# Kernel optimization log

Hardware: AMD Instinct MI355X
Metric: run time of the kernel (lower is better)

## Reference

```python
import jax, jax.numpy as jnp
import numpy as np

N_NODES = 100000
N_EDGES = 1600000
IN_C, HID_C, OUT_C = 64, 64, 32


def setup_inputs() -> dict:
    key = jax.random.key(0)
    ks = jax.random.split(key, 10)
    return {
        "x": jax.random.normal(ks[0], (N_NODES, IN_C), dtype=jnp.float32),
        "edge_index": jax.random.randint(ks[1], (2, N_EDGES), 0, N_NODES, dtype=jnp.int32),
        "W_l": jax.random.normal(ks[2], (IN_C, HID_C), dtype=jnp.float32) * 0.1,
        "W_r": jax.random.normal(ks[3], (IN_C, HID_C), dtype=jnp.float32) * 0.1,
        "b1": jax.random.normal(ks[4], (HID_C,), dtype=jnp.float32) * 0.1,
        "W_g": jax.random.normal(ks[5], (HID_C, OUT_C), dtype=jnp.float32) * 0.1,
        "att_src": jax.random.normal(ks[6], (OUT_C,), dtype=jnp.float32) * 0.1,
        "att_dst": jax.random.normal(ks[7], (OUT_C,), dtype=jnp.float32) * 0.1,
        "b2": jax.random.normal(ks[8], (OUT_C,), dtype=jnp.float32) * 0.1,
    }


def _gnn(x, edge_index, W_l, W_r, b1, W_g, att_src, att_dst, b2):
    n = x.shape[0]
    src, dst = edge_index[0], edge_index[1]

    # --- SAGEConv: mean neighbor aggregation + root transform ---
    deg = jax.ops.segment_sum(jnp.ones_like(src, dtype=x.dtype), dst, num_segments=n)
    agg = jax.ops.segment_sum(x[src], dst, num_segments=n)  # [N, IN_C]
    agg = agg / jnp.maximum(deg, 1.0)[:, None]
    h = agg @ W_l + b1 + x @ W_r
    h = jax.nn.relu(h)
    # dropout(p=0.5) is identity in eval mode

    # --- GATConv (heads=1), with self-loops (PyG default) ---
    loop = jnp.arange(n, dtype=src.dtype)
    s = jnp.concatenate([src, loop])
    d = jnp.concatenate([dst, loop])
    z = h @ W_g                      # [N, OUT_C]
    a_s = z @ att_src                # [N] per-node source score
    a_d = z @ att_dst                # [N] per-node dest score
    e = jax.nn.leaky_relu(a_s[s] + a_d[d], negative_slope=0.2)  # [E+N]
    # segment softmax over edges grouped by destination node
    m = jax.ops.segment_max(e, d, num_segments=n)
    ex = jnp.exp(e - m[d])
    denom = jax.ops.segment_sum(ex, d, num_segments=n)
    alpha = ex / denom[d]
    out = jax.ops.segment_sum(alpha[:, None] * z[s], d, num_segments=n) + b2

    return jax.nn.log_softmax(out, axis=1)


def reference(x, edge_index, W_l, W_r, b1, W_g, att_src, att_dst, b2):
    return _gnn(x, edge_index, W_l, W_r, b1, W_g, att_src, att_dst, b2)
```

## Files before the change

kernel.cpp:

```cpp
#include <hip/hip_runtime.h>
#include <cstdint>
#include <cstddef>


typedef unsigned short ushort_t;
typedef unsigned int uint_t;
typedef __attribute__((ext_vector_type(8))) short short8;
typedef __attribute__((ext_vector_type(4))) float f32x4;
typedef __attribute__((ext_vector_type(2))) float f32x2;

__device__ inline ushort_t f2bf(float f) {
    uint_t u = __float_as_uint(f);
    uint_t r = (u + 0x7fffu + ((u >> 16) & 1u)) >> 16;
    return (ushort_t)r;
}
__device__ inline uint_t pkbf(float a, float b) {
    return (uint_t)f2bf(a) | ((uint_t)f2bf(b) << 16);
}

#define PART_CHUNK 8192


__global__ __launch_bounds__(256) void k_pre(const float* __restrict__ x, ushort_t* __restrict__ xh,
                                             unsigned char* __restrict__ xq,
                                             const int* __restrict__ ei,
                                             int* __restrict__ cnt,
                                             const float* __restrict__ Wl, const float* __restrict__ Wr,
                                             const float* __restrict__ Wg,
                                             ushort_t* __restrict__ Wlrt, ushort_t* __restrict__ Wgt,
                                             unsigned char* __restrict__ zq,
                                             int n4, int E, int NB, int N, int nchunk) {
    __shared__ int h[512];
    int bid = blockIdx.x, tid = threadIdx.x;
    int idx = bid * 256 + tid;
    if (idx < n4) {
        float4 v = ((const float4*)x)[idx];
        ushort4 o = { f2bf(v.x), f2bf(v.y), f2bf(v.z), f2bf(v.w) };
        ((ushort4*)xh)[idx] = o;
        int r = 0;
        r = __builtin_amdgcn_cvt_pk_fp8_f32(v.x, v.y, r, false);
        r = __builtin_amdgcn_cvt_pk_fp8_f32(v.z, v.w, r, true);
        ((uint_t*)xq)[idx] = (uint_t)r;
    }
    if (bid < nchunk) {
        for (int b = tid; b < NB; b += 256) h[b] = 0;
        __syncthreads();
        int b0 = bid * PART_CHUNK;
        int b1 = min(b0 + PART_CHUNK, E);
        for (int j = b0 + tid; j < b1; j += 256) atomicAdd(&h[ei[E + j] >> 8], 1);
        __syncthreads();
        int* crow = cnt + (size_t)bid * NB;
        for (int b = tid; b < NB; b += 256) crow[b] = h[b];
    } else if (bid == nchunk) {
        if (tid < 16) ((uint_t*)(xq + (size_t)N * 64))[tid] = 0;
        if (tid < 8)  ((uint_t*)(zq + (size_t)N * 32))[tid] = 0;
    } else if (bid >= 512 && bid < 544) {
        int t = (bid - 512) * 256 + tid;
        int n = t >> 7, k = t & 127;
        float v = (k < 64) ? Wl[k * 64 + n] : Wr[(k - 64) * 64 + n];
        Wlrt[n * 128 + k] = f2bf(v);
        if (t < 32 * 64) {
            int n2 = t >> 6, k2 = t & 63;
            Wgt[n2 * 64 + k2] = f2bf(Wg[k2 * 32 + n2]);
        }
    }
}


__global__ __launch_bounds__(256) void k_part(const int* __restrict__ ei, const int* __restrict__ cnt,
                                              int* __restrict__ base, int* __restrict__ rowptr,
                                              uint_t* __restrict__ pairs, int E, int NB, int N,
                                              int nchunk) {
    __shared__ int tot_s[512];
    __shared__ int ofs[512];
    __shared__ int t[256];
    int tid = threadIdx.x, bid = blockIdx.x;
    for (int b = tid; b < NB; b += 256) {
        const int* col = cnt + b;
        int tsum = 0, moff = 0;
        int c = 0;
        for (; c + 16 <= nchunk; c += 16) {
            int v[16];
            #pragma unroll
            for (int k = 0; k < 16; ++k) v[k] = col[(size_t)(c + k) * NB];
            #pragma unroll
            for (int k = 0; k < 16; ++k) {
                tsum += v[k];
                moff += (c + k < bid) ? v[k] : 0;
            }
        }
        for (; c < nchunk; ++c) {
            int v = col[(size_t)c * NB];
            tsum += v;
            moff += (c < bid) ? v : 0;
        }
        tot_s[b] = tsum;
        ofs[b] = moff;
    }
    __syncthreads();
    int v0 = (2 * tid < NB) ? tot_s[2 * tid] : 0;
    int v1 = (2 * tid + 1 < NB) ? tot_s[2 * tid + 1] : 0;
    t[tid] = v0 + v1;
    __syncthreads();
    for (int off = 1; off < 256; off <<= 1) {
        int u = (tid >= off) ? t[tid - off] : 0;
        __syncthreads();
        t[tid] += u;
        __syncthreads();
    }
    int pairExcl = (tid > 0) ? t[tid - 1] : 0;
    if (2 * tid < NB) {
        ofs[2 * tid] += pairExcl;
        if (bid == 0) base[2 * tid] = pairExcl;
    }
    if (2 * tid + 1 < NB) {
        ofs[2 * tid + 1] += pairExcl + v0;
        if (bid == 0) base[2 * tid + 1] = pairExcl + v0;
    }
    if (bid == 0 && tid == 0) { base[NB] = E; rowptr[N] = E; }
    __syncthreads();
    int b0 = bid * PART_CHUNK;
    int b1 = min(b0 + PART_CHUNK, E);
    for (int j = b0 + tid; j < b1; j += 256) {
        int d = ei[E + j], s = ei[j];
        int p = atomicAdd(&ofs[d >> 8], 1);
        pairs[p] = (uint_t)s | ((uint_t)(d & 255) << 24);
    }
}


__global__ __launch_bounds__(256) void k_csr(const uint_t* __restrict__ pairs, const int* __restrict__ base,
                                             int* __restrict__ rowptr, int* __restrict__ csr, int N) {
    __shared__ int h[256];
    __shared__ int s[256];
    int b = blockIdx.x;
    int d0 = b << 8;
    int e0 = base[b], e1 = base[b + 1];
    int tid = threadIdx.x;
    h[tid] = 0;
    __syncthreads();
    for (int j = e0 + tid; j < e1; j += 256) atomicAdd(&h[pairs[j] >> 24], 1);
    __syncthreads();
    int v = h[tid];
    s[tid] = v;
    __syncthreads();
    for (int off = 1; off < 256; off <<= 1) {
        int u = (tid >= off) ? s[tid - off] : 0;
        __syncthreads();
        s[tid] += u;
        __syncthreads();
    }
    int excl = s[tid] - v;
    if (d0 + tid < N) rowptr[d0 + tid] = e0 + excl;
    __syncthreads();
    h[tid] = e0 + excl;
    __syncthreads();
    for (int j = e0 + tid; j < e1; j += 256) {
        uint_t p = pairs[j];
        int pos = atomicAdd(&h[p >> 24], 1);
        csr[pos] = (int)(p & 0xffffffu);
    }
}


__global__ __launch_bounds__(256) void k_gather(const int* __restrict__ rowptr, const int* __restrict__ csr,
                                                const unsigned char* __restrict__ xq,
                                                ushort_t* __restrict__ aggh, int N) {
    __shared__ int scr[256];
    int tid = threadIdx.x;
    int l = tid & 15, g = tid >> 4;
    int i = blockIdx.x * 16 + g;
    if (i >= N) return;
    int r0 = rowptr[i], r1 = rowptr[i + 1];
    int sub = l >> 3, lc = l & 7;
    const char* xb = (const char*)xq + lc * 8;
    float a0 = 0.f, a1 = 0.f, a2 = 0.f, a3 = 0.f;
    float a4 = 0.f, a5 = 0.f, a6 = 0.f, a7 = 0.f;
    for (int bb = r0; bb < r1; bb += 16) {
        int idx = bb + l;
        int src = (idx < r1) ? csr[idx] : N;
        scr[tid] = src << 6;
        uint4 q0 = *(const uint4*)&scr[g * 16 + 0];
        uint4 q1 = *(const uint4*)&scr[g * 16 + 4];
        uint4 q2 = *(const uint4*)&scr[g * 16 + 8];
        uint4 q3 = *(const uint4*)&scr[g * 16 + 12];
#define HSTEP(oa, ob) { \
        uint_t off = sub ? (ob) : (oa); \
        uint2 u = *(const uint2*)(xb + off); \
        f32x2 p0 = __builtin_amdgcn_cvt_pk_f32_fp8((int)u.x, false); \
        f32x2 p1 = __builtin_amdgcn_cvt_pk_f32_fp8((int)u.x, true); \
        f32x2 p2 = __builtin_amdgcn_cvt_pk_f32_fp8((int)u.y, false); \
        f32x2 p3 = __builtin_amdgcn_cvt_pk_f32_fp8((int)u.y, true); \
        a0 += p0.x; a1 += p0.y; a2 += p1.x; a3 += p1.y; \
        a4 += p2.x; a5 += p2.y; a6 += p3.x; a7 += p3.y; }
        HSTEP(q0.x, q0.y) HSTEP(q0.z, q0.w)
        HSTEP(q1.x, q1.y) HSTEP(q1.z, q1.w)
        HSTEP(q2.x, q2.y) HSTEP(q2.z, q2.w)
        HSTEP(q3.x, q3.y) HSTEP(q3.z, q3.w)
#undef HSTEP
    }
    a0 += __shfl_xor(a0, 8, 64); a1 += __shfl_xor(a1, 8, 64);
    a2 += __shfl_xor(a2, 8, 64); a3 += __shfl_xor(a3, 8, 64);
    a4 += __shfl_xor(a4, 8, 64); a5 += __shfl_xor(a5, 8, 64);
    a6 += __shfl_xor(a6, 8, 64); a7 += __shfl_xor(a7, 8, 64);
    if (sub == 0) {
        float dn = 1.0f / fmaxf((float)(r1 - r0), 1.0f);
        uint4 o = { pkbf(a0 * dn, a1 * dn), pkbf(a2 * dn, a3 * dn),
                    pkbf(a4 * dn, a5 * dn), pkbf(a6 * dn, a7 * dn) };
        *(uint4*)(aggh + (size_t)i * 64 + lc * 8) = o;
    }
}


__global__ __launch_bounds__(256) void k_gemm(const ushort_t* __restrict__ aggh, const ushort_t* __restrict__ xh,
                                              const ushort_t* __restrict__ Wlrt, const ushort_t* __restrict__ Wgt,
                                              const float* __restrict__ b1,
                                              const float* __restrict__ att_src, const float* __restrict__ att_dst,
                                              unsigned char* __restrict__ zq, float* __restrict__ a_s,
                                              float* __restrict__ a_d, int N) {
    __shared__ ushort_t Wls[64 * 136];
    __shared__ ushort_t Wgs[32 * 72];
    __shared__ ushort_t hs[64 * 136];
    int tid = threadIdx.x;
    for (int t = tid; t < 64 * 16; t += 256) {
        int n = t >> 4, cq = t & 15;
        *(uint4*)(&Wls[n * 136 + cq * 8]) = *(const uint4*)(&Wlrt[n * 128 + cq * 8]);
    }
    for (int t = tid; t < 32 * 8; t += 256) {
        int n = t >> 3, cq = t & 7;
        *(uint4*)(&Wgs[n * 72 + cq * 8]) = *(const uint4*)(&Wgt[n * 64 + cq * 8]);
    }
    __syncthreads();

    int w = tid >> 6, lane = tid & 63;
    int c = lane & 15, quad = lane >> 4;
    int m0 = blockIdx.x * 64 + w * 16;
    int row = m0 + c;
    bool rowok = row < N;

    f32x4 acc[4] = {};
    #pragma unroll
    for (int kk = 0; kk < 4; ++kk) {
        const ushort_t* Abase = (kk < 2) ? aggh : xh;
        int koff = (kk & 1) * 32 + quad * 8;
        short8 a = {};
        if (rowok) a = *(const short8*)(Abase + (size_t)row * 64 + koff);
        #pragma unroll
        for (int nb = 0; nb < 4; ++nb) {
            short8 b = *(const short8*)(&Wls[(nb * 16 + c) * 136 + kk * 32 + quad * 8]);
            acc[nb] = __builtin_amdgcn_mfma_f32_16x16x32_bf16(a, b, acc[nb], 0, 0, 0);
        }
    }
    ushort_t* hw = &hs[w * 16 * 136];
    #pragma unroll
    for (int nb = 0; nb < 4; ++nb) {
        float bb = b1[nb * 16 + c];
        #pragma unroll
        for (int r = 0; r < 4; ++r) {
            float h = acc[nb][r] + bb;
            hw[(quad * 4 + r) * 136 + nb * 16 + c] = f2bf(fmaxf(h, 0.f));
        }
    }
    f32x4 acc2[2] = {};
    #pragma unroll
    for (int kk = 0; kk < 2; ++kk) {
        short8 a = *(const short8*)(&hw[c * 136 + kk * 32 + quad * 8]);
        #pragma unroll
        for (int nb = 0; nb < 2; ++nb) {
            short8 b = *(const short8*)(&Wgs[(nb * 16 + c) * 72 + kk * 32 + quad * 8]);
            acc2[nb] = __builtin_amdgcn_mfma_f32_16x16x32_bf16(a, b, acc2[nb], 0, 0, 0);
        }
    }
    float as0 = att_src[c], as1 = att_src[16 + c];
    float ad0 = att_dst[c], ad1 = att_dst[16 + c];
    #pragma unroll
    for (int r = 0; r < 4; ++r) {
        int grow = m0 + quad * 4 + r;
        float z0 = acc2[0][r], z1 = acc2[1][r];
        float ps = z0 * as0 + z1 * as1;
        float pd = z0 * ad0 + z1 * ad1;
        #pragma unroll
        for (int off = 8; off; off >>= 1) {
            ps += __shfl_xor(ps, off, 64);
            pd += __shfl_xor(pd, off, 64);
        }
        if (grow < N) {
            int r8 = __builtin_amdgcn_cvt_pk_fp8_f32(z0, z1, 0, false);
            unsigned char* zrow = zq + (size_t)grow * 32;
            zrow[c] = (unsigned char)(r8 & 0xff);
            zrow[16 + c] = (unsigned char)((r8 >> 8) & 0xff);
            if (c == 0) { a_s[grow] = ps; a_d[grow] = pd; }
        }
    }
}


__global__ __launch_bounds__(256) void k_gat(const unsigned char* __restrict__ zq, const float* __restrict__ a_s,
                                             const float* __restrict__ a_d, const int* __restrict__ rowptr,
                                             const int* __restrict__ csr, const float* __restrict__ b2,
                                             float* __restrict__ out, int N) {
    __shared__ uint2 scr[256];
    int tid = threadIdx.x;
    int l = tid & 15, g = tid >> 4;
    int i = blockIdx.x * 16 + g;
    if (i >= N) return;
    int r0 = rowptr[i], r1 = rowptr[i + 1];
    float adi = a_d[i], asi = a_s[i];
    int sub = l >> 3, lc = l & 7;
    const char* zb = (const char*)zq + lc * 4;
    float a0 = 0.f, a1 = 0.f, a2 = 0.f, a3 = 0.f, dsum = 0.f;

    for (int bb = r0; bb < r1; bb += 16) {
        int idx = bb + l;
        bool valid = idx < r1;
        int s_l = valid ? csr[idx] : N;
        float w_l = 0.f;
        if (valid) {
            float e = a_s[s_l] + adi;
            e = fmaxf(e, 0.2f * e);
            w_l = __expf(e);
            dsum += w_l;
        }
        scr[tid] = make_uint2((uint_t)(s_l << 5), __float_as_uint(w_l));
        #pragma unroll
        for (int r = 0; r < 8; ++r) {
            uint4 q = *(const uint4*)&scr[g * 16 + r * 2];
            uint_t off = sub ? q.z : q.x;
            float w = __uint_as_float(sub ? q.w : q.y);
            uint_t u = *(const uint_t*)(zb + off);
            f32x2 p0 = __builtin_amdgcn_cvt_pk_f32_fp8((int)u, false);
            f32x2 p1 = __builtin_amdgcn_cvt_pk_f32_fp8((int)u, true);
            a0 += w * p0.x; a1 += w * p0.y;
            a2 += w * p1.x; a3 += w * p1.y;
        }
    }
    #pragma unroll
    for (int off = 8; off; off >>= 1) dsum += __shfl_xor(dsum, off, 64);
    a0 += __shfl_xor(a0, 8, 64); a1 += __shfl_xor(a1, 8, 64);
    a2 += __shfl_xor(a2, 8, 64); a3 += __shfl_xor(a3, 8, 64);
    float es = asi + adi; es = fmaxf(es, 0.2f * es);
    float wse = __expf(es);
    float denom = dsum + wse;
    uint_t us = *(const uint_t*)((const char*)zq + (size_t)i * 32 + lc * 4);
    f32x2 s0 = __builtin_amdgcn_cvt_pk_f32_fp8((int)us, false);
    f32x2 s1 = __builtin_amdgcn_cvt_pk_f32_fp8((int)us, true);
    a0 += wse * s0.x; a1 += wse * s0.y;
    a2 += wse * s1.x; a3 += wse * s1.y;

    float rden = 1.0f / denom;
    float o0 = a0 * rden + b2[lc * 4 + 0];
    float o1 = a1 * rden + b2[lc * 4 + 1];
    float o2 = a2 * rden + b2[lc * 4 + 2];
    float o3 = a3 * rden + b2[lc * 4 + 3];
    float m2 = fmaxf(fmaxf(o0, o1), fmaxf(o2, o3));
    #pragma unroll
    for (int off = 4; off; off >>= 1) m2 = fmaxf(m2, __shfl_xor(m2, off, 64));
    float ssum = __expf(o0 - m2) + __expf(o1 - m2) + __expf(o2 - m2) + __expf(o3 - m2);
    #pragma unroll
    for (int off = 4; off; off >>= 1) ssum += __shfl_xor(ssum, off, 64);
    float lg = m2 + __logf(ssum);
    if (sub == 0) {
        float4 r = { o0 - lg, o1 - lg, o2 - lg, o3 - lg };
        *(float4*)(out + (size_t)i * 32 + lc * 4) = r;
    }
}


extern "C" void kernel_launch(void* const* d_in, const int* in_sizes, int n_in,
                              void* d_out, int out_size, void* d_ws, size_t ws_size,
                              hipStream_t stream) {
    const float* x       = (const float*)d_in[0];
    const int*   ei      = (const int*)d_in[1];
    const float* Wl      = (const float*)d_in[2];
    const float* Wr      = (const float*)d_in[3];
    const float* b1      = (const float*)d_in[4];
    const float* Wg      = (const float*)d_in[5];
    const float* att_src = (const float*)d_in[6];
    const float* att_dst = (const float*)d_in[7];
    const float* b2      = (const float*)d_in[8];
    float* out = (float*)d_out;

    int N = in_sizes[0] / 64;
    int E = in_sizes[1] / 2;
    int NB = (N + 255) >> 8;
    int nchunk = (E + PART_CHUNK - 1) / PART_CHUNK;

    char* ws = (char*)d_ws;
    size_t off = 0;
    auto alloc = [&](size_t bytes) { size_t r = off; off += (bytes + 255) & ~(size_t)255; return r; };
    int* base      = (int*)(ws + alloc((size_t)(NB + 1) * 4));
    int* cnt       = (int*)(ws + alloc((size_t)nchunk * NB * 4));
    int* rowptr    = (int*)(ws + alloc((size_t)(N + 1) * 4));
    uint_t* pairs  = (uint_t*)(ws + alloc((size_t)E * 4));
    int* csr       = (int*)(ws + alloc((size_t)E * 4));
    ushort_t* xh   = (ushort_t*)(ws + alloc((size_t)N * 64 * 2));
    unsigned char* xq = (unsigned char*)(ws + alloc((size_t)(N + 1) * 64));
    ushort_t* aggh = (ushort_t*)(ws + alloc((size_t)N * 64 * 2));
    unsigned char* zq = (unsigned char*)(ws + alloc((size_t)(N + 1) * 32));
    float* a_s     = (float*)(ws + alloc((size_t)N * 4));
    float* a_d     = (float*)(ws + alloc((size_t)N * 4));
    ushort_t* Wlrt = (ushort_t*)(ws + alloc(64 * 128 * 2));
    ushort_t* Wgt  = (ushort_t*)(ws + alloc(32 * 64 * 2));

    int n4 = N * 64 / 4;
    int gpre = (n4 + 255) / 256;
    if (gpre < 545) gpre = 545;
    k_pre    <<<gpre, 256, 0, stream>>>(x, xh, xq, ei, cnt, Wl, Wr, Wg, Wlrt, Wgt, zq, n4, E, NB, N, nchunk);
    k_part   <<<nchunk, 256, 0, stream>>>(ei, cnt, base, rowptr, pairs, E, NB, N, nchunk);
    k_csr    <<<NB, 256, 0, stream>>>(pairs, base, rowptr, csr, N);
    k_gather <<<(N + 15) / 16, 256, 0, stream>>>(rowptr, csr, xq, aggh, N);
    k_gemm   <<<(N + 63) / 64, 256, 0, stream>>>(aggh, xh, Wlrt, Wgt, b1, att_src, att_dst, zq, a_s, a_d, N);
    k_gat    <<<(N + 15) / 16, 256, 0, stream>>>(zq, a_s, a_d, rowptr, csr, b2, out, N);
}
```

Baseline: 194.3 us.

## Fuse neighbor-mean gather into SAGE GEMM kernel via shared-memory aggregate

Merges the gather kernel into the GEMM kernel. Each 64-row block now computes its own neighbor means into shared memory and feeds them straight to the MFMA stage, removing the bf16 aggregate buffer and its global write and read, plus one launch. The cost is less parallelism in the gather phase: 64 nodes per block instead of 16, so there are four times fewer blocks. Load imbalance across degrees also now stalls the GEMM part of the same block.

```diff
diff --git a/kernel.cpp b/kernel.cpp
--- a/kernel.cpp
+++ b/kernel.cpp
@@ -163,65 +163,21 @@
 }
 
 
-__global__ __launch_bounds__(256) void k_gather(const int* __restrict__ rowptr, const int* __restrict__ csr,
-                                                const unsigned char* __restrict__ xq,
-                                                ushort_t* __restrict__ aggh, int N) {
-    __shared__ int scr[256];
-    int tid = threadIdx.x;
-    int l = tid & 15, g = tid >> 4;
-    int i = blockIdx.x * 16 + g;
-    if (i >= N) return;
-    int r0 = rowptr[i], r1 = rowptr[i + 1];
-    int sub = l >> 3, lc = l & 7;
-    const char* xb = (const char*)xq + lc * 8;
-    float a0 = 0.f, a1 = 0.f, a2 = 0.f, a3 = 0.f;
-    float a4 = 0.f, a5 = 0.f, a6 = 0.f, a7 = 0.f;
-    for (int bb = r0; bb < r1; bb += 16) {
-        int idx = bb + l;
-        int src = (idx < r1) ? csr[idx] : N;
-        scr[tid] = src << 6;
-        uint4 q0 = *(const uint4*)&scr[g * 16 + 0];
-        uint4 q1 = *(const uint4*)&scr[g * 16 + 4];
-        uint4 q2 = *(const uint4*)&scr[g * 16 + 8];
-        uint4 q3 = *(const uint4*)&scr[g * 16 + 12];
-#define HSTEP(oa, ob) { \
-        uint_t off = sub ? (ob) : (oa); \
-        uint2 u = *(const uint2*)(xb + off); \
-        f32x2 p0 = __builtin_amdgcn_cvt_pk_f32_fp8((int)u.x, false); \
-        f32x2 p1 = __builtin_amdgcn_cvt_pk_f32_fp8((int)u.x, true); \
-        f32x2 p2 = __builtin_amdgcn_cvt_pk_f32_fp8((int)u.y, false); \
-        f32x2 p3 = __builtin_amdgcn_cvt_pk_f32_fp8((int)u.y, true); \
-        a0 += p0.x; a1 += p0.y; a2 += p1.x; a3 += p1.y; \
-        a4 += p2.x; a5 += p2.y; a6 += p3.x; a7 += p3.y; }
-        HSTEP(q0.x, q0.y) HSTEP(q0.z, q0.w)
-        HSTEP(q1.x, q1.y) HSTEP(q1.z, q1.w)
-        HSTEP(q2.x, q2.y) HSTEP(q2.z, q2.w)
-        HSTEP(q3.x, q3.y) HSTEP(q3.z, q3.w)
-#undef HSTEP
-    }
-    a0 += __shfl_xor(a0, 8, 64); a1 += __shfl_xor(a1, 8, 64);
-    a2 += __shfl_xor(a2, 8, 64); a3 += __shfl_xor(a3, 8, 64);
-    a4 += __shfl_xor(a4, 8, 64); a5 += __shfl_xor(a5, 8, 64);
-    a6 += __shfl_xor(a6, 8, 64); a7 += __shfl_xor(a7, 8, 64);
-    if (sub == 0) {
-        float dn = 1.0f / fmaxf((float)(r1 - r0), 1.0f);
-        uint4 o = { pkbf(a0 * dn, a1 * dn), pkbf(a2 * dn, a3 * dn),
-                    pkbf(a4 * dn, a5 * dn), pkbf(a6 * dn, a7 * dn) };
-        *(uint4*)(aggh + (size_t)i * 64 + lc * 8) = o;
-    }
-}
-
-
-__global__ __launch_bounds__(256) void k_gemm(const ushort_t* __restrict__ aggh, const ushort_t* __restrict__ xh,
-                                              const ushort_t* __restrict__ Wlrt, const ushort_t* __restrict__ Wgt,
-                                              const float* __restrict__ b1,
-                                              const float* __restrict__ att_src, const float* __restrict__ att_dst,
-                                              unsigned char* __restrict__ zq, float* __restrict__ a_s,
-                                              float* __restrict__ a_d, int N) {
+__global__ __launch_bounds__(256) void k_gg(const int* __restrict__ rowptr, const int* __restrict__ csr,
+                                            const unsigned char* __restrict__ xq,
+                                            const ushort_t* __restrict__ xh,
+                                            const ushort_t* __restrict__ Wlrt, const ushort_t* __restrict__ Wgt,
+                                            const float* __restrict__ b1,
+                                            const float* __restrict__ att_src, const float* __restrict__ att_dst,
+                                            unsigned char* __restrict__ zq, float* __restrict__ a_s,
+                                            float* __restrict__ a_d, int N) {
     __shared__ ushort_t Wls[64 * 136];
     __shared__ ushort_t Wgs[32 * 72];
-    __shared__ ushort_t hs[64 * 136];
+    __shared__ ushort_t agg[64 * 72];
+    __shared__ __align__(16) char hsraw[64 * 136 * 2];
     int tid = threadIdx.x;
+    int blk = blockIdx.x;
+
     for (int t = tid; t < 64 * 16; t += 256) {
         int n = t >> 4, cq = t & 15;
         *(uint4*)(&Wls[n * 136 + cq * 8]) = *(const uint4*)(&Wlrt[n * 128 + cq * 8]);
@@ -230,21 +186,74 @@
         int n = t >> 3, cq = t & 7;
         *(uint4*)(&Wgs[n * 72 + cq * 8]) = *(const uint4*)(&Wgt[n * 64 + cq * 8]);
     }
-    __syncthreads();
-
+
+    {
+        int* scr = (int*)hsraw;
+        int l = tid & 15, g = tid >> 4;
+        int sub = l >> 3, lc = l & 7;
+        const char* xb = (const char*)xq + lc * 8;
+        #pragma unroll
+        for (int rep = 0; rep < 4; ++rep) {
+            int ilocal = rep * 16 + g;
+            int i = blk * 64 + ilocal;
+            if (i < N) {
+                int r0 = rowptr[i], r1 = rowptr[i + 1];
+                float a0 = 0.f, a1 = 0.f, a2 = 0.f, a3 = 0.f;
+                float a4 = 0.f, a5 = 0.f, a6 = 0.f, a7 = 0.f;
+                for (int bb = r0; bb < r1; bb += 16) {
+                    int idx = bb + l;
+                    int src = (idx < r1) ? csr[idx] : N;
+                    scr[tid] = src << 6;
+                    uint4 q0 = *(const uint4*)&scr[g * 16 + 0];
+                    uint4 q1 = *(const uint4*)&scr[g * 16 + 4];
+                    uint4 q2 = *(const uint4*)&scr[g * 16 + 8];
+                    uint4 q3 = *(const uint4*)&scr[g * 16 + 12];
+#define HSTEP(oa, ob) { \
+                    uint_t off = sub ? (ob) : (oa); \
+                    uint2 u = *(const uint2*)(xb + off); \
+                    f32x2 p0 = __builtin_amdgcn_cvt_pk_f32_fp8((int)u.x, false); \
+                    f32x2 p1 = __builtin_amdgcn_cvt_pk_f32_fp8((int)u.x, true); \
+                    f32x2 p2 = __builtin_amdgcn_cvt_pk_f32_fp8((int)u.y, false); \
+                    f32x2 p3 = __builtin_amdgcn_cvt_pk_f32_fp8((int)u.y, true); \
+                    a0 += p0.x; a1 += p0.y; a2 += p1.x; a3 += p1.y; \
+                    a4 += p2.x; a5 += p2.y; a6 += p3.x; a7 += p3.y; }
+                    HSTEP(q0.x, q0.y) HSTEP(q0.z, q0.w)
+                    HSTEP(q1.x, q1.y) HSTEP(q1.z, q1.w)
+                    HSTEP(q2.x, q2.y) HSTEP(q2.z, q2.w)
+                    HSTEP(q3.x, q3.y) HSTEP(q3.z, q3.w)
+#undef HSTEP
+                }
+                a0 += __shfl_xor(a0, 8, 64); a1 += __shfl_xor(a1, 8, 64);
+                a2 += __shfl_xor(a2, 8, 64); a3 += __shfl_xor(a3, 8, 64);
+                a4 += __shfl_xor(a4, 8, 64); a5 += __shfl_xor(a5, 8, 64);
+                a6 += __shfl_xor(a6, 8, 64); a7 += __shfl_xor(a7, 8, 64);
+                if (sub == 0) {
+                    float dn = 1.0f / fmaxf((float)(r1 - r0), 1.0f);
+                    uint4 o = { pkbf(a0 * dn, a1 * dn), pkbf(a2 * dn, a3 * dn),
+                                pkbf(a4 * dn, a5 * dn), pkbf(a6 * dn, a7 * dn) };
+                    *(uint4*)(&agg[ilocal * 72 + lc * 8]) = o;
+                }
+            }
+        }
+    }
+    __syncthreads();
+
+    ushort_t* hs = (ushort_t*)hsraw;
     int w = tid >> 6, lane = tid & 63;
     int c = lane & 15, quad = lane >> 4;
-    int m0 = blockIdx.x * 64 + w * 16;
+    int m0 = blk * 64 + w * 16;
     int row = m0 + c;
     bool rowok = row < N;
 
     f32x4 acc[4] = {};
     #pragma unroll
     for (int kk = 0; kk < 4; ++kk) {
-        const ushort_t* Abase = (kk < 2) ? aggh : xh;
         int koff = (kk & 1) * 32 + quad * 8;
         short8 a = {};
-        if (rowok) a = *(const short8*)(Abase + (size_t)row * 64 + koff);
+        if (rowok) {
+            if (kk < 2) a = *(const short8*)(&agg[(w * 16 + c) * 72 + koff]);
+            else        a = *(const short8*)(xh + (size_t)row * 64 + koff);
+        }
         #pragma unroll
         for (int nb = 0; nb < 4; ++nb) {
             short8 b = *(const short8*)(&Wls[(nb * 16 + c) * 136 + kk * 32 + quad * 8]);
@@ -395,7 +404,6 @@
     int* csr       = (int*)(ws + alloc((size_t)E * 4));
     ushort_t* xh   = (ushort_t*)(ws + alloc((size_t)N * 64 * 2));
     unsigned char* xq = (unsigned char*)(ws + alloc((size_t)(N + 1) * 64));
-    ushort_t* aggh = (ushort_t*)(ws + alloc((size_t)N * 64 * 2));
     unsigned char* zq = (unsigned char*)(ws + alloc((size_t)(N + 1) * 32));
     float* a_s     = (float*)(ws + alloc((size_t)N * 4));
     float* a_d     = (float*)(ws + alloc((size_t)N * 4));
@@ -405,10 +413,9 @@
     int n4 = N * 64 / 4;
     int gpre = (n4 + 255) / 256;
     if (gpre < 545) gpre = 545;
-    k_pre    <<<gpre, 256, 0, stream>>>(x, xh, xq, ei, cnt, Wl, Wr, Wg, Wlrt, Wgt, zq, n4, E, NB, N, nchunk);
-    k_part   <<<nchunk, 256, 0, stream>>>(ei, cnt, base, rowptr, pairs, E, NB, N, nchunk);
-    k_csr    <<<NB, 256, 0, stream>>>(pairs, base, rowptr, csr, N);
-    k_gather <<<(N + 15) / 16, 256, 0, stream>>>(rowptr, csr, xq, aggh, N);
-    k_gemm   <<<(N + 63) / 64, 256, 0, stream>>>(aggh, xh, Wlrt, Wgt, b1, att_src, att_dst, zq, a_s, a_d, N);
-    k_gat    <<<(N + 15) / 16, 256, 0, stream>>>(zq, a_s, a_d, rowptr, csr, b2, out, N);
-}
+    k_pre  <<<gpre, 256, 0, stream>>>(x, xh, xq, ei, cnt, Wl, Wr, Wg, Wlrt, Wgt, zq, n4, E, NB, N, nchunk);
+    k_part <<<nchunk, 256, 0, stream>>>(ei, cnt, base, rowptr, pairs, E, NB, N, nchunk);
+    k_csr  <<<NB, 256, 0, stream>>>(pairs, base, rowptr, csr, N);
+    k_gg   <<<(N + 63) / 64, 256, 0, stream>>>(rowptr, csr, xq, xh, Wlrt, Wgt, b1, att_src, att_dst, zq, a_s, a_d, N);
+    k_gat  <<<(N + 15) / 16, 256, 0, stream>>>(zq, a_s, a_d, rowptr, csr, b2, out, N);
+}
```

After: 202.7 us. 1.04x slower.
